# Performance work log

Hardware: AMD Instinct MI355X
Metric: run time of the kernel (lower is better)

Reference implementation:

```python
import jax, jax.numpy as jnp
import numpy as np

NUM_HEADS = 8
NEG_MASK = -1000.0  # original code masks with -1000, not -inf


def setup_inputs() -> dict:
    key = jax.random.key(0)
    ks = jax.random.split(key, 12)
    B, S, D = 4, 2048, 512
    HID, OUT = 512, 512
    dh = D // NUM_HEADS      # 64, per-head input dim
    eh = HID // NUM_HEADS    # 64, per-head hidden dim
    w = 0.02
    return {
        "q": jax.random.normal(ks[0], (B, S, D), dtype=jnp.float32),
        "k": jax.random.normal(ks[1], (B, S, D), dtype=jnp.float32),
        "v": jax.random.normal(ks[2], (B, S, D), dtype=jnp.float32),
        # Linear weights stored as [in, out] (transpose of torch convention)
        "Wq": jax.random.normal(ks[3], (dh, eh), dtype=jnp.float32) * w,
        "bq": jax.random.normal(ks[4], (eh,), dtype=jnp.float32) * w,
        "Wk": jax.random.normal(ks[5], (dh, eh), dtype=jnp.float32) * w,
        "bk": jax.random.normal(ks[6], (eh,), dtype=jnp.float32) * w,
        "Wv": jax.random.normal(ks[7], (dh, eh), dtype=jnp.float32) * w,
        "bv": jax.random.normal(ks[8], (eh,), dtype=jnp.float32) * w,
        "Wo": jax.random.normal(ks[9], (HID, OUT), dtype=jnp.float32) * w,
        "bo": jax.random.normal(ks[10], (OUT,), dtype=jnp.float32) * w,
        "valid_lens": jnp.maximum(jax.random.randint(ks[11], (B,), 0, S), 1),
        "max_len": S,
    }


def reference(q, k, v, Wq, bq, Wk, bk, Wv, bv, Wo, bo, valid_lens, max_len):
    B, S, D = q.shape
    H = NUM_HEADS
    # split into heads: [B, S, H, dh]; note the SAME projection weights are
    # shared across heads (as in the original module)
    qh = q.reshape(B, S, H, D // H)
    kh = k.reshape(B, S, H, D // H)
    vh = v.reshape(B, S, H, D // H)
    qp = jnp.einsum('bshd,de->bshe', qh, Wq) + bq  # [B,S,H,eh]
    kp = jnp.einsum('bshd,de->bshe', kh, Wk) + bk
    vp = jnp.einsum('bshd,de->bshe', vh, Wv) + bv
    scale = 1.0 / jnp.sqrt(jnp.asarray(qp.shape[-1], qp.dtype))
    scores = jnp.einsum('bshe,bthe->bhst', qp, kp) * scale  # [B,H,S,S]
    # key-padding mask: positions j >= valid_len get -1000 (original semantics)
    key_mask = jnp.arange(S)[None, :] < valid_lens[:, None]  # [B,S]
    scores = jnp.where(key_mask[:, None, None, :], scores, NEG_MASK)
    attn = jax.nn.softmax(scores, axis=-1)
    ctx = jnp.einsum('bhst,bthe->bshe', attn, vp).reshape(B, S, -1)  # head-major concat
    return jnp.einsum('bse,eo->bso', ctx, Wo) + bo
```

## Files before the change

kernel.cpp:

```cpp
#include <hip/hip_runtime.h>

#define S_LEN 2048
#define D_MODEL 512

typedef __attribute__((ext_vector_type(8))) short s8v;
typedef __attribute__((ext_vector_type(4))) float f4v;
typedef __attribute__((ext_vector_type(4))) short s4v;
typedef __attribute__((ext_vector_type(4))) int   i4v;
typedef __attribute__((ext_vector_type(2))) int   i2v;

#define MFMA __builtin_amdgcn_mfma_f32_16x16x32_bf16

__device__ inline short f2bf(float x) {
    union { float f; unsigned u; } v; v.f = x;
    unsigned r = v.u + 0x7fffu + ((v.u >> 16) & 1u);
    return (short)(r >> 16);
}
__device__ inline unsigned pack_bf2_trunc(float a, float b) {
    unsigned ua = __builtin_bit_cast(unsigned, a);
    unsigned ub = __builtin_bit_cast(unsigned, b);
    return (ua >> 16) | (ub & 0xffff0000u);
}

template <int C>
__device__ inline float dppf(float x) {
    int i = __builtin_bit_cast(int, x);
    i = __builtin_amdgcn_update_dpp(0, i, C, 0xF, 0xF, true);
    return __builtin_bit_cast(float, i);
}
__device__ inline float rowsum16(float x) {
    x += dppf<0xB1>(x);
    x += dppf<0x4E>(x);
    x += dppf<0x141>(x);
    x += dppf<0x140>(x);
    return x;
}

typedef const __attribute__((address_space(1))) void* gptr_t;
typedef __attribute__((address_space(3))) void* sptr_t;
__device__ inline void gload16(const void* g, void* s) {
    __builtin_amdgcn_global_load_lds((gptr_t)g, (sptr_t)s, 16, 0, 0);
}

__global__ __launch_bounds__(256) void prep_kernel(
    const float* __restrict__ Wo, const float* __restrict__ Wq,
    const float* __restrict__ Wk, const float* __restrict__ Wv,
    short* __restrict__ WoT, short* __restrict__ WqT,
    short* __restrict__ WkT, short* __restrict__ WvT)
{
    if (blockIdx.x < 64) {
        __shared__ short t[64 * 65];
        const int bi = (blockIdx.x >> 3) * 64;
        const int bj = (blockIdx.x & 7) * 64;
        const int c = threadIdx.x & 63, rr = threadIdx.x >> 6;
#pragma unroll
        for (int r = 0; r < 16; r++) {
            int i = r * 4 + rr;
            t[c * 65 + i] = f2bf(Wo[(size_t)(bi + i) * 512 + bj + c]);
        }
        __syncthreads();
#pragma unroll
        for (int r = 0; r < 16; r++) {
            int o = r * 4 + rr;
            WoT[(size_t)(bj + o) * 512 + bi + c] = t[o * 65 + c];
        }
    } else {
        for (int j = threadIdx.x; j < 12288; j += 256) {
            int w = j >> 12, r = j & 4095;
            int e = r >> 6, d = r & 63;
            const float* W = (w == 0) ? Wq : (w == 1) ? Wk : Wv;
            short* WT = (w == 0) ? WqT : (w == 1) ? WkT : WvT;
            WT[r] = f2bf(W[d * 64 + e]);
        }
    }
}

__global__ __launch_bounds__(256) void proj_kernel(
    const float* __restrict__ q, const float* __restrict__ k, const float* __restrict__ v,
    const float* __restrict__ bq, const float* __restrict__ bk, const float* __restrict__ bv,
    const short* __restrict__ WqT, const short* __restrict__ WkT, const short* __restrict__ WvT,
    short* __restrict__ qp, short* __restrict__ kp, short* __restrict__ vpT)
{
    const int t = blockIdx.z >> 2;
    const int b = blockIdx.z & 3;
    const int h = blockIdx.y;
    const int qt = blockIdx.x;
    const int w = threadIdx.x >> 6, lane = threadIdx.x & 63;
    const int l = lane & 15, qd = lane >> 4;

    const float* X    = (t == 0) ? q   : (t == 1) ? k   : v;
    const float* bias = (t == 0) ? bq  : (t == 1) ? bk  : bv;
    const short* WT   = (t == 0) ? WqT : (t == 1) ? WkT : WvT;

    const int s0 = qt * 128 + w * 32;

    s8v a[2][2];
#pragma unroll
    for (int mt = 0; mt < 2; mt++)
#pragma unroll
        for (int kk = 0; kk < 2; kk++) {
            const float* p = X + (size_t)(b * S_LEN + s0 + mt * 16 + l) * 512 + h * 64 + kk * 32 + qd * 8;
            f4v x0 = *(const f4v*)p;
            f4v x1 = *(const f4v*)(p + 4);
            s8v fr;
            fr[0] = f2bf(x0[0]); fr[1] = f2bf(x0[1]); fr[2] = f2bf(x0[2]); fr[3] = f2bf(x0[3]);
            fr[4] = f2bf(x1[0]); fr[5] = f2bf(x1[1]); fr[6] = f2bf(x1[2]); fr[7] = f2bf(x1[3]);
            a[mt][kk] = fr;
        }
    s8v wf[4][2];
#pragma unroll
    for (int nt = 0; nt < 4; nt++) {
        int wrow = (t < 2) ? (4 * l + nt) : (nt * 16 + l);
#pragma unroll
        for (int kk = 0; kk < 2; kk++)
            wf[nt][kk] = *(const s8v*)(WT + wrow * 64 + kk * 32 + qd * 8);
    }

    const f4v fz = {0.f, 0.f, 0.f, 0.f};
    f4v acc[2][4];
#pragma unroll
    for (int mt = 0; mt < 2; mt++)
#pragma unroll
        for (int nt = 0; nt < 4; nt++) acc[mt][nt] = fz;

#pragma unroll
    for (int kk = 0; kk < 2; kk++)
#pragma unroll
        for (int nt = 0; nt < 4; nt++)
#pragma unroll
            for (int mt = 0; mt < 2; mt++)
                acc[mt][nt] = MFMA(a[mt][kk], wf[nt][kk], acc[mt][nt], 0, 0, 0);

    const float SC = 0.125f * 1.442695041f;

    if (t < 2) {
        short* out = (t == 0) ? qp : kp;
        float bbs[4];
#pragma unroll
        for (int nt = 0; nt < 4; nt++) bbs[nt] = bias[4 * l + nt];
#pragma unroll
        for (int mt = 0; mt < 2; mt++)
#pragma unroll
            for (int r = 0; r < 4; r++) {
                int s = s0 + mt * 16 + qd * 4 + r;
                s4v pk;
#pragma unroll
                for (int nt = 0; nt < 4; nt++) {
                    float val = acc[mt][nt][r] + bbs[nt];
                    if (t == 0) val *= SC;
                    pk[nt] = f2bf(val);
                }
                *(s4v*)(out + ((size_t)(b * 8 + h) * S_LEN + s) * 64 + 4 * l) = pk;
            }
    } else {
#pragma unroll
        for (int nt = 0; nt < 4; nt++) {
            float bb = bias[nt * 16 + l];
            int e = nt * 16 + l;
#pragma unroll
            for (int mt = 0; mt < 2; mt++) {
                s4v pk;
#pragma unroll
                for (int r = 0; r < 4; r++) pk[r] = f2bf(acc[mt][nt][r] + bb);
                *(s4v*)(vpT + ((size_t)(b * 8 + h) * 64 + e) * S_LEN + s0 + mt * 16 + qd * 4) = pk;
            }
        }
    }
}

__global__ __launch_bounds__(128) void repack_kernel(
    const short* __restrict__ kp, const short* __restrict__ vpT,
    short* __restrict__ kfrag, short* __restrict__ vfrag)
{
    const int kb = blockIdx.x, h = blockIdx.y, b = blockIdx.z;
    const int bh = b * 8 + h;
    const int half = threadIdx.x >> 6, f = threadIdx.x & 63;
    const int l = f & 15, qd = f >> 4;
    const size_t slab = (size_t)bh * S_LEN * 64;
    const size_t obase = ((size_t)bh * 32 + kb) * 4096;
    if (half == 0) {
        const short* src = kp + slab;
#pragma unroll
        for (int c = 0; c < 8; c++) {
            int nt = c >> 1, kk = c & 1;
            s8v x = *(const s8v*)(src + (size_t)(kb * 64 + 4 * l + nt) * 64 + kk * 32 + qd * 8);
            *(s8v*)(kfrag + obase + c * 512 + f * 8) = x;
        }
    } else {
        const short* src = vpT + slab;
#pragma unroll
        for (int c = 0; c < 8; c++) {
            int ne = c >> 1, kk = c & 1;
            s8v x = *(const s8v*)(src + (size_t)(4 * l + ne) * S_LEN + kb * 64 + kk * 32 + qd * 8);
            *(s8v*)(vfrag + obase + c * 512 + f * 8) = x;
        }
    }
}

__global__ __launch_bounds__(256, 3) void attn_kernel(
    const short* __restrict__ qp, const short* __restrict__ kfrag,
    const short* __restrict__ vfrag,
    const int* __restrict__ valid_lens, short* __restrict__ ctx)
{
    __shared__ alignas(16) short kbuf[2][4096];
    __shared__ alignas(16) short vbuf[2][4096];
    __shared__ alignas(16) short lP[4][32 * 72];

    const int gid = blockIdx.x;
    const int h  = gid & 7;
    int b        = (gid >> 3) & 3;
    const int qt = gid >> 5;
    b ^= 3 * ((gid >> 8) & 1);
    const int w = threadIdx.x >> 6, lane = threadIdx.x & 63;
    const int l = lane & 15, qd = lane >> 4;
    const int vlen = valid_lens[b];
    const int ntiles = (vlen + 63) >> 6;

    const int bh = b * 8 + h;
    const short* Qs = qp + (size_t)bh * S_LEN * 64;
    const short* Kf = kfrag + (size_t)bh * 32 * 4096;
    const short* Vf = vfrag + (size_t)bh * 32 * 4096;

    const int s0 = qt * 128 + w * 32;
    s8v qf[2][2];
#pragma unroll
    for (int mt = 0; mt < 2; mt++)
#pragma unroll
        for (int kk = 0; kk < 2; kk++)
            qf[mt][kk] = *(const s8v*)(Qs + (size_t)(s0 + mt * 16 + l) * 64 + kk * 32 + qd * 8);

    const f4v fz = {0.f, 0.f, 0.f, 0.f};
    f4v O[2][4];
    float lsum[2][4];
#pragma unroll
    for (int mt = 0; mt < 2; mt++)
#pragma unroll
        for (int r = 0; r < 4; r++) lsum[mt][r] = 0.f;
#pragma unroll
    for (int mt = 0; mt < 2; mt++)
#pragma unroll
        for (int ne = 0; ne < 4; ne++) O[mt][ne] = fz;

    short* lPw = lP[w];
    const int toff = threadIdx.x * 8;

    gload16(Kf + toff,        &kbuf[0][toff]);
    gload16(Kf + 2048 + toff, &kbuf[0][2048 + toff]);
    gload16(Vf + toff,        &vbuf[0][toff]);
    gload16(Vf + 2048 + toff, &vbuf[0][2048 + toff]);
    __syncthreads();

    for (int kb = 0; kb < ntiles; kb++) {
        const int cur = kb & 1;
        if (kb + 1 < ntiles) {
            const short* Ks = Kf + (size_t)(kb + 1) * 4096;
            const short* Vs = Vf + (size_t)(kb + 1) * 4096;
            gload16(Ks + toff,        &kbuf[cur ^ 1][toff]);
            gload16(Ks + 2048 + toff, &kbuf[cur ^ 1][2048 + toff]);
            gload16(Vs + toff,        &vbuf[cur ^ 1][toff]);
            gload16(Vs + 2048 + toff, &vbuf[cur ^ 1][2048 + toff]);
        }

        const short* Kb = &kbuf[cur][lane * 8];
        s8v kf[4][2];
#pragma unroll
        for (int nt = 0; nt < 4; nt++)
#pragma unroll
            for (int kk = 0; kk < 2; kk++)
                kf[nt][kk] = *(const s8v*)(Kb + (nt * 2 + kk) * 512);

        f4v sf[2][4];
#pragma unroll
        for (int mt = 0; mt < 2; mt++)
#pragma unroll
            for (int nt = 0; nt < 4; nt++) sf[mt][nt] = fz;
        __builtin_amdgcn_s_setprio(1);
#pragma unroll
        for (int nt = 0; nt < 4; nt++)
#pragma unroll
            for (int mt = 0; mt < 2; mt++) {
                sf[mt][nt] = MFMA(qf[mt][0], kf[nt][0], sf[mt][nt], 0, 0, 0);
                sf[mt][nt] = MFMA(qf[mt][1], kf[nt][1], sf[mt][nt], 0, 0, 0);
            }
        __builtin_amdgcn_s_setprio(0);

        const short* Vb = &vbuf[cur][lane * 8];
        s8v vf[4][2];
#pragma unroll
        for (int ne = 0; ne < 4; ne++)
#pragma unroll
            for (int kk = 0; kk < 2; kk++)
                vf[ne][kk] = *(const s8v*)(Vb + (ne * 2 + kk) * 512);

        if (kb == ntiles - 1 && (vlen & 63)) {
            int rem = vlen - kb * 64;
#pragma unroll
            for (int nt = 0; nt < 4; nt++)
                if (4 * l + nt >= rem) {
#pragma unroll
                    for (int mt = 0; mt < 2; mt++)
#pragma unroll
                        for (int r = 0; r < 4; r++) sf[mt][nt][r] = -1e30f;
                }
        }

#pragma unroll
        for (int mt = 0; mt < 2; mt++)
#pragma unroll
            for (int r = 0; r < 4; r++) {
                float p0 = __builtin_amdgcn_exp2f(sf[mt][0][r]);
                float p1 = __builtin_amdgcn_exp2f(sf[mt][1][r]);
                float p2 = __builtin_amdgcn_exp2f(sf[mt][2][r]);
                float p3 = __builtin_amdgcn_exp2f(sf[mt][3][r]);
                lsum[mt][r] += (p0 + p1) + (p2 + p3);
                i2v pk;
                pk[0] = (int)pack_bf2_trunc(p0, p1);
                pk[1] = (int)pack_bf2_trunc(p2, p3);
                *(i2v*)(lPw + (mt * 16 + qd * 4 + r) * 72 + 4 * l) = pk;
            }

        s8v pa[2][2];
#pragma unroll
        for (int mt = 0; mt < 2; mt++)
#pragma unroll
            for (int kk = 0; kk < 2; kk++)
                pa[mt][kk] = *(const s8v*)(lPw + (mt * 16 + l) * 72 + kk * 32 + qd * 8);
        __builtin_amdgcn_s_setprio(1);
#pragma unroll
        for (int ne = 0; ne < 4; ne++)
#pragma unroll
            for (int mt = 0; mt < 2; mt++) {
                O[mt][ne] = MFMA(pa[mt][0], vf[ne][0], O[mt][ne], 0, 0, 0);
                O[mt][ne] = MFMA(pa[mt][1], vf[ne][1], O[mt][ne], 0, 0, 0);
            }
        __builtin_amdgcn_s_setprio(0);

        __syncthreads();
    }

#pragma unroll
    for (int mt = 0; mt < 2; mt++)
#pragma unroll
        for (int r = 0; r < 4; r++) {
            float inv = 1.0f / rowsum16(lsum[mt][r]);
            int s = s0 + mt * 16 + qd * 4 + r;
            s4v pk;
#pragma unroll
            for (int ne = 0; ne < 4; ne++) pk[ne] = f2bf(O[mt][ne][r] * inv);
            *(s4v*)(ctx + ((size_t)(b * S_LEN + s)) * 512 + h * 64 + 4 * l) = pk;
        }
}

__global__ __launch_bounds__(256) void outproj_kernel(
    const short* __restrict__ ctx, const short* __restrict__ WoT,
    const float* __restrict__ bo, float* __restrict__ out)
{
    __shared__ short lB[64 * 520];
    __shared__ short lA[128 * 40];

    const int rb = blockIdx.x * 128;
    const int nb = blockIdx.y * 64;
    const int w = threadIdx.x >> 6, lane = threadIdx.x & 63;
    const int l = lane & 15, qd = lane >> 4;

    {
        int n = threadIdx.x >> 2, c0 = threadIdx.x & 3;
#pragma unroll
        for (int i = 0; i < 16; i++) {
            int g = i * 4 + c0;
            i4v x = *(const i4v*)(WoT + (size_t)(nb + n) * 512 + g * 8);
            *(i4v*)(lB + n * 520 + g * 8) = x;
        }
    }
    __syncthreads();

    const f4v fz = {0.f, 0.f, 0.f, 0.f};
    f4v acc[2][4];
#pragma unroll
    for (int mt = 0; mt < 2; mt++)
#pragma unroll
        for (int nt = 0; nt < 4; nt++) acc[mt][nt] = fz;

    for (int ko = 0; ko < 16; ko++) {
        {
            int r = threadIdx.x >> 1, hp = threadIdx.x & 1;
            const short* src = ctx + (size_t)(rb + r) * 512 + ko * 32 + hp * 16;
            i4v x0 = *(const i4v*)src;
            i4v x1 = *(const i4v*)(src + 8);
            *(i4v*)(lA + r * 40 + hp * 16) = x0;
            *(i4v*)(lA + r * 40 + hp * 16 + 8) = x1;
        }
        __syncthreads();
        s8v af[2];
#pragma unroll
        for (int mt = 0; mt < 2; mt++)
            af[mt] = *(const s8v*)(lA + (w * 32 + mt * 16 + l) * 40 + qd * 8);
#pragma unroll
        for (int nt = 0; nt < 4; nt++) {
            s8v bfr = *(const s8v*)(lB + (nt * 16 + l) * 520 + ko * 32 + qd * 8);
#pragma unroll
            for (int mt = 0; mt < 2; mt++)
                acc[mt][nt] = MFMA(af[mt], bfr, acc[mt][nt], 0, 0, 0);
        }
        __syncthreads();
    }

#pragma unroll
    for (int nt = 0; nt < 4; nt++) {
        float bias = bo[nb + nt * 16 + l];
#pragma unroll
        for (int mt = 0; mt < 2; mt++)
#pragma unroll
            for (int r = 0; r < 4; r++) {
                int row = rb + w * 32 + mt * 16 + qd * 4 + r;
                out[(size_t)row * 512 + nb + nt * 16 + l] = acc[mt][nt][r] + bias;
            }
    }
}

extern "C" void kernel_launch(void* const* d_in, const int* in_sizes, int n_in,
                              void* d_out, int out_size, void* d_ws, size_t ws_size,
                              hipStream_t stream)
{
    const float* q  = (const float*)d_in[0];
    const float* k  = (const float*)d_in[1];
    const float* v  = (const float*)d_in[2];
    const float* Wq = (const float*)d_in[3];
    const float* bq = (const float*)d_in[4];
    const float* Wk = (const float*)d_in[5];
    const float* bk = (const float*)d_in[6];
    const float* Wv = (const float*)d_in[7];
    const float* bv = (const float*)d_in[8];
    const float* Wo = (const float*)d_in[9];
    const float* bo = (const float*)d_in[10];
    const int*   vl = (const int*)d_in[11];
    float* out = (float*)d_out;

    char* ws = (char*)d_ws;
    const size_t SL = (size_t)4 * 8 * S_LEN * 64 * sizeof(short);
    short* qp    = (short*)(ws);
    short* kp    = (short*)(ws + SL);
    short* ctx   = (short*)(ws + SL);
    short* vpT   = (short*)(ws + 2 * SL);
    short* kfrag = (short*)(ws + 3 * SL);
    short* vfrag = (short*)(ws + 4 * SL);
    short* WoT = (short*)(ws + 5 * SL);
    short* WqT = WoT + 512 * 512;
    short* WkT = WqT + 4096;
    short* WvT = WkT + 4096;

    prep_kernel<<<65, 256, 0, stream>>>(Wo, Wq, Wk, Wv, WoT, WqT, WkT, WvT);
    proj_kernel<<<dim3(16, 8, 12), 256, 0, stream>>>(q, k, v, bq, bk, bv,
                                                     WqT, WkT, WvT, qp, kp, vpT);
    repack_kernel<<<dim3(32, 8, 4), 128, 0, stream>>>(kp, vpT, kfrag, vfrag);
    attn_kernel<<<512, 256, 0, stream>>>(qp, kfrag, vfrag, vl, ctx);
    outproj_kernel<<<dim3(64, 8), 256, 0, stream>>>(ctx, WoT, bo, out);
}
```

Before: 180.3 us.

## Fuse K/V repack into projection kernel via swizzled LDS staging

The projection kernel now converts and transposes the per-head Wq/Wk/Wv weights into swizzled shared memory itself, instead of relying on the prep kernel. It also writes K and V directly in the MFMA fragment layout by staging the tile through LDS, which removes the separate repack kernel and the intermediate kp/vpT global buffers. This saves one launch and a global round trip of K/V. In exchange, every projection block redundantly converts a 64x64 weight and pays extra barriers and LDS traffic.

Measured after the change: 165.3 us. 1.09x faster.

```diff
diff --git a/kernel.cpp b/kernel.cpp
--- a/kernel.cpp
+++ b/kernel.cpp
@@ -43,44 +43,33 @@
 }
 
 __global__ __launch_bounds__(256) void prep_kernel(
-    const float* __restrict__ Wo, const float* __restrict__ Wq,
-    const float* __restrict__ Wk, const float* __restrict__ Wv,
-    short* __restrict__ WoT, short* __restrict__ WqT,
-    short* __restrict__ WkT, short* __restrict__ WvT)
+    const float* __restrict__ Wo, short* __restrict__ WoT)
 {
-    if (blockIdx.x < 64) {
-        __shared__ short t[64 * 65];
-        const int bi = (blockIdx.x >> 3) * 64;
-        const int bj = (blockIdx.x & 7) * 64;
-        const int c = threadIdx.x & 63, rr = threadIdx.x >> 6;
-#pragma unroll
-        for (int r = 0; r < 16; r++) {
-            int i = r * 4 + rr;
-            t[c * 65 + i] = f2bf(Wo[(size_t)(bi + i) * 512 + bj + c]);
-        }
-        __syncthreads();
-#pragma unroll
-        for (int r = 0; r < 16; r++) {
-            int o = r * 4 + rr;
-            WoT[(size_t)(bj + o) * 512 + bi + c] = t[o * 65 + c];
-        }
-    } else {
-        for (int j = threadIdx.x; j < 12288; j += 256) {
-            int w = j >> 12, r = j & 4095;
-            int e = r >> 6, d = r & 63;
-            const float* W = (w == 0) ? Wq : (w == 1) ? Wk : Wv;
-            short* WT = (w == 0) ? WqT : (w == 1) ? WkT : WvT;
-            WT[r] = f2bf(W[d * 64 + e]);
-        }
+    __shared__ short t[64 * 65];
+    const int bi = (blockIdx.x >> 3) * 64;
+    const int bj = (blockIdx.x & 7) * 64;
+    const int c = threadIdx.x & 63, rr = threadIdx.x >> 6;
+#pragma unroll
+    for (int r = 0; r < 16; r++) {
+        int i = r * 4 + rr;
+        t[c * 65 + i] = f2bf(Wo[(size_t)(bi + i) * 512 + bj + c]);
+    }
+    __syncthreads();
+#pragma unroll
+    for (int r = 0; r < 16; r++) {
+        int o = r * 4 + rr;
+        WoT[(size_t)(bj + o) * 512 + bi + c] = t[o * 65 + c];
     }
 }
 
 __global__ __launch_bounds__(256) void proj_kernel(
     const float* __restrict__ q, const float* __restrict__ k, const float* __restrict__ v,
+    const float* __restrict__ Wq, const float* __restrict__ Wk, const float* __restrict__ Wv,
     const float* __restrict__ bq, const float* __restrict__ bk, const float* __restrict__ bv,
-    const short* __restrict__ WqT, const short* __restrict__ WkT, const short* __restrict__ WvT,
-    short* __restrict__ qp, short* __restrict__ kp, short* __restrict__ vpT)
+    short* __restrict__ qp, short* __restrict__ kfrag, short* __restrict__ vfrag)
 {
+    __shared__ short sm[128 * 64];
+
     const int t = blockIdx.z >> 2;
     const int b = blockIdx.z & 3;
     const int h = blockIdx.y;
@@ -88,9 +77,27 @@
     const int w = threadIdx.x >> 6, lane = threadIdx.x & 63;
     const int l = lane & 15, qd = lane >> 4;
 
-    const float* X    = (t == 0) ? q   : (t == 1) ? k   : v;
-    const float* bias = (t == 0) ? bq  : (t == 1) ? bk  : bv;
-    const short* WT   = (t == 0) ? WqT : (t == 1) ? WkT : WvT;
+    const float* X    = (t == 0) ? q  : (t == 1) ? k  : v;
+    const float* Wp   = (t == 0) ? Wq : (t == 1) ? Wk : Wv;
+    const float* bias = (t == 0) ? bq : (t == 1) ? bk : bv;
+
+    {
+        const int d = threadIdx.x >> 2, c4 = threadIdx.x & 3;
+        const float* src = Wp + d * 64 + c4 * 16;
+        f4v x0 = *(const f4v*)(src);
+        f4v x1 = *(const f4v*)(src + 4);
+        f4v x2 = *(const f4v*)(src + 8);
+        f4v x3 = *(const f4v*)(src + 12);
+        float xs[16] = {x0[0],x0[1],x0[2],x0[3], x1[0],x1[1],x1[2],x1[3],
+                        x2[0],x2[1],x2[2],x2[3], x3[0],x3[1],x3[2],x3[3]};
+#pragma unroll
+        for (int j = 0; j < 16; j++) {
+            int e = c4 * 16 + j;
+            int sidx = (e * 64 + d) ^ (((e >> 2) & 7) << 3);
+            sm[sidx] = f2bf(xs[j]);
+        }
+    }
+    __syncthreads();
 
     const int s0 = qt * 128 + w * 32;
 
@@ -111,9 +118,10 @@
 #pragma unroll
     for (int nt = 0; nt < 4; nt++) {
         int wrow = (t < 2) ? (4 * l + nt) : (nt * 16 + l);
+        int key = ((wrow >> 2) & 7) << 3;
 #pragma unroll
         for (int kk = 0; kk < 2; kk++)
-            wf[nt][kk] = *(const s8v*)(WT + wrow * 64 + kk * 32 + qd * 8);
+            wf[nt][kk] = *(const s8v*)(sm + ((wrow * 64 + kk * 32 + qd * 8) ^ key));
     }
 
     const f4v fz = {0.f, 0.f, 0.f, 0.f};
@@ -133,8 +141,7 @@
 
     const float SC = 0.125f * 1.442695041f;
 
-    if (t < 2) {
-        short* out = (t == 0) ? qp : kp;
+    if (t == 0) {
         float bbs[4];
 #pragma unroll
         for (int nt = 0; nt < 4; nt++) bbs[nt] = bias[4 * l + nt];
@@ -145,56 +152,69 @@
                 int s = s0 + mt * 16 + qd * 4 + r;
                 s4v pk;
 #pragma unroll
-                for (int nt = 0; nt < 4; nt++) {
-                    float val = acc[mt][nt][r] + bbs[nt];
-                    if (t == 0) val *= SC;
-                    pk[nt] = f2bf(val);
-                }
-                *(s4v*)(out + ((size_t)(b * 8 + h) * S_LEN + s) * 64 + 4 * l) = pk;
+                for (int nt = 0; nt < 4; nt++)
+                    pk[nt] = f2bf((acc[mt][nt][r] + bbs[nt]) * SC);
+                *(s4v*)(qp + ((size_t)(b * 8 + h) * S_LEN + s) * 64 + 4 * l) = pk;
+            }
+        return;
+    }
+
+    __syncthreads();
+
+    if (t == 1) {
+        float bbs[4];
+#pragma unroll
+        for (int nt = 0; nt < 4; nt++) bbs[nt] = bias[4 * l + nt];
+#pragma unroll
+        for (int mt = 0; mt < 2; mt++)
+#pragma unroll
+            for (int r = 0; r < 4; r++) {
+                int sl = w * 32 + mt * 16 + qd * 4 + r;
+                s4v pk;
+#pragma unroll
+                for (int nt = 0; nt < 4; nt++) pk[nt] = f2bf(acc[mt][nt][r] + bbs[nt]);
+                int sidx = (sl * 64 + 4 * l) ^ (((sl >> 2) & 7) << 3);
+                *(s4v*)(sm + sidx) = pk;
             }
     } else {
 #pragma unroll
         for (int nt = 0; nt < 4; nt++) {
             float bb = bias[nt * 16 + l];
             int e = nt * 16 + l;
+            int key = ((e >> 2) & 7) << 3;
 #pragma unroll
             for (int mt = 0; mt < 2; mt++) {
                 s4v pk;
 #pragma unroll
                 for (int r = 0; r < 4; r++) pk[r] = f2bf(acc[mt][nt][r] + bb);
-                *(s4v*)(vpT + ((size_t)(b * 8 + h) * 64 + e) * S_LEN + s0 + mt * 16 + qd * 4) = pk;
-            }
-        }
-    }
-}
-
-__global__ __launch_bounds__(128) void repack_kernel(
-    const short* __restrict__ kp, const short* __restrict__ vpT,
-    short* __restrict__ kfrag, short* __restrict__ vfrag)
-{
-    const int kb = blockIdx.x, h = blockIdx.y, b = blockIdx.z;
-    const int bh = b * 8 + h;
-    const int half = threadIdx.x >> 6, f = threadIdx.x & 63;
-    const int l = f & 15, qd = f >> 4;
-    const size_t slab = (size_t)bh * S_LEN * 64;
-    const size_t obase = ((size_t)bh * 32 + kb) * 4096;
-    if (half == 0) {
-        const short* src = kp + slab;
-#pragma unroll
-        for (int c = 0; c < 8; c++) {
-            int nt = c >> 1, kk = c & 1;
-            s8v x = *(const s8v*)(src + (size_t)(kb * 64 + 4 * l + nt) * 64 + kk * 32 + qd * 8);
-            *(s8v*)(kfrag + obase + c * 512 + f * 8) = x;
-        }
-    } else {
-        const short* src = vpT + slab;
-#pragma unroll
-        for (int c = 0; c < 8; c++) {
-            int ne = c >> 1, kk = c & 1;
-            s8v x = *(const s8v*)(src + (size_t)(4 * l + ne) * S_LEN + kb * 64 + kk * 32 + qd * 8);
-            *(s8v*)(vfrag + obase + c * 512 + f * 8) = x;
-        }
-    }
+                int sidx = (e * 128 + w * 32 + mt * 16 + qd * 4) ^ key;
+                *(s4v*)(sm + sidx) = pk;
+            }
+        }
+    }
+    __syncthreads();
+
+    short* dst = (t == 1) ? kfrag : vfrag;
+    const size_t obase0 = ((size_t)(b * 8 + h) * 32 + qt * 2) * 4096;
+    const int f = threadIdx.x & 63, cp = threadIdx.x >> 6;
+    const int fl = f & 15, fq = f >> 4;
+#pragma unroll
+    for (int tt = 0; tt < 2; tt++)
+#pragma unroll
+        for (int ci = 0; ci < 2; ci++) {
+            int c = cp + ci * 4;
+            int n2 = c >> 1, kk = c & 1;
+            int sidx;
+            if (t == 1) {
+                int sl = tt * 64 + 4 * fl + n2;
+                sidx = (sl * 64 + kk * 32 + fq * 8) ^ (((sl >> 2) & 7) << 3);
+            } else {
+                int e = 4 * fl + n2;
+                sidx = (e * 128 + tt * 64 + kk * 32 + fq * 8) ^ (((e >> 2) & 7) << 3);
+            }
+            s8v x = *(const s8v*)(sm + sidx);
+            *(s8v*)(dst + obase0 + tt * 4096 + c * 512 + f * 8) = x;
+        }
 }
 
 __global__ __launch_bounds__(256, 3) void attn_kernel(
@@ -439,20 +459,14 @@
     char* ws = (char*)d_ws;
     const size_t SL = (size_t)4 * 8 * S_LEN * 64 * sizeof(short);
     short* qp    = (short*)(ws);
-    short* kp    = (short*)(ws + SL);
     short* ctx   = (short*)(ws + SL);
-    short* vpT   = (short*)(ws + 2 * SL);
-    short* kfrag = (short*)(ws + 3 * SL);
-    short* vfrag = (short*)(ws + 4 * SL);
-    short* WoT = (short*)(ws + 5 * SL);
-    short* WqT = WoT + 512 * 512;
-    short* WkT = WqT + 4096;
-    short* WvT = WkT + 4096;
-
-    prep_kernel<<<65, 256, 0, stream>>>(Wo, Wq, Wk, Wv, WoT, WqT, WkT, WvT);
-    proj_kernel<<<dim3(16, 8, 12), 256, 0, stream>>>(q, k, v, bq, bk, bv,
-                                                     WqT, WkT, WvT, qp, kp, vpT);
-    repack_kernel<<<dim3(32, 8, 4), 128, 0, stream>>>(kp, vpT, kfrag, vfrag);
+    short* kfrag = (short*)(ws + 2 * SL);
+    short* vfrag = (short*)(ws + 3 * SL);
+    short* WoT   = (short*)(ws + 4 * SL);
+
+    prep_kernel<<<64, 256, 0, stream>>>(Wo, WoT);
+    proj_kernel<<<dim3(16, 8, 12), 256, 0, stream>>>(q, k, v, Wq, Wk, Wv,
+                                                     bq, bk, bv, qp, kfrag, vfrag);
     attn_kernel<<<512, 256, 0, stream>>>(qp, kfrag, vfrag, vl, ctx);
     outproj_kernel<<<dim3(64, 8), 256, 0, stream>>>(ctx, WoT, bo, out);
 }
```
